# Performance work log

Measured on AMD Instinct MI355X. Metric: run time of the kernel, lower is better.

Reference implementation:

```python
import jax, jax.numpy as jnp
import numpy as np

EPS = 1e-5

def _branch(x, W, gamma, beta):
    # 1x1 conv (no bias) + InstanceNorm2d(affine) + ReLU
    y = jnp.einsum('oc,bchw->bohw', W, x)
    mu = y.mean(axis=(2, 3), keepdims=True)
    var = y.var(axis=(2, 3), keepdims=True)
    y = (y - mu) * jax.lax.rsqrt(var + EPS)
    y = y * gamma[None, :, None, None] + beta[None, :, None, None]
    return jax.nn.relu(y)

def setup_inputs() -> dict:
    key = jax.random.key(0)
    ks = jax.random.split(key, 12)
    b, in_ch, h, w = 2, 256, 64, 64
    c = in_ch // 8
    d = dict(
        x1=jax.random.normal(ks[0], (b, in_ch, h, w), jnp.float32),
        x2=jax.random.normal(ks[1], (b, in_ch, h, w), jnp.float32),
        x3=jax.random.normal(ks[2], (b, in_ch, h, w), jnp.float32),
        W1=jax.random.normal(ks[3], (c, in_ch), jnp.float32) * (1.0 / np.sqrt(in_ch)),
        g1=jnp.ones((c,), jnp.float32), b1=jnp.zeros((c,), jnp.float32),
        W2=jax.random.normal(ks[4], (c, in_ch), jnp.float32) * (1.0 / np.sqrt(in_ch)),
        g2=jnp.ones((c,), jnp.float32), b2=jnp.zeros((c,), jnp.float32),
        W3=jax.random.normal(ks[5], (c, in_ch), jnp.float32) * (1.0 / np.sqrt(in_ch)),
        g3=jnp.ones((c,), jnp.float32), b3=jnp.zeros((c,), jnp.float32),
    )
    return d

def _forward(x1, x2, x3, W1, g1, b1, W2, g2, b2, W3, g3, b3):
    q1 = _branch(x1, W1, g1, b1); q2 = _branch(x2, W1, g1, b1); q3 = _branch(x3, W1, g1, b1)
    k1 = _branch(x1, W2, g2, b2); k2 = _branch(x2, W2, g2, b2); k3 = _branch(x3, W2, g2, b2)
    v1 = _branch(x1, W3, g3, b3); v2 = _branch(x2, W3, g3, b3); v3 = _branch(x3, W3, g3, b3)
    b_, c, h, w = q1.shape
    hw = h * w
    Q1 = q1.reshape(b_, c, hw).transpose(0, 2, 1)  # [b,hw,c]
    Q2 = q2.reshape(b_, c, hw).transpose(0, 2, 1)
    Q3 = q3.reshape(b_, c, hw).transpose(0, 2, 1)
    K1 = k1.reshape(b_, c, hw)                      # [b,c,hw]
    K2 = k2.reshape(b_, c, hw)
    K3 = k3.reshape(b_, c, hw)
    sm = lambda Q, K: jax.nn.softmax(jnp.einsum('bic,bcj->bij', Q, K), axis=-1)
    A12 = sm(Q1, K2); A21 = sm(Q2, K1); A23 = sm(Q2, K3)
    A32 = sm(Q3, K2); A13 = sm(Q1, K3)
    # ones[b,c,hw] @ A == broadcast of column-sums of A: track a [b,hw] vector
    colsum = lambda A: A.sum(axis=1)                        # [b,hw]
    step = lambda v, A: jnp.einsum('bk,bkj->bj', v, A)      # [b,hw]
    def bc(v):  # broadcast [b,hw] -> [b,c,h,w]
        return jnp.broadcast_to(v[:, None, :], (b_, c, hw)).reshape(b_, c, h, w)
    p1a = bc(step(step(step(colsum(A12), A23), A32), A21))
    p1b = bc(step(colsum(A12), A21))
    p2 = bc(step(colsum(A23), A32))
    p3a = bc(step(colsum(A12), A23))
    p3b = bc(colsum(A13))
    return (p1a, p1b, p2, p3a, p3b, v1, v2, v3)

def reference(x1, x2, x3, W1, g1, b1, W2, g2, b2, W3, g3, b3):
    return _forward(x1, x2, x3, W1, g1, b1, W2, g2, b2, W3, g3, b3)
```

## Files before the change

### kernel.cpp

```cpp
#include <hip/hip_runtime.h>

typedef unsigned short u16;
typedef u16  u16x8  __attribute__((ext_vector_type(8)));
typedef _Float16 f16x4 __attribute__((ext_vector_type(4)));
typedef _Float16 f16x8 __attribute__((ext_vector_type(8)));
typedef float f32x4 __attribute__((ext_vector_type(4)));

#define HW 4096
#define CIN 256
#define HW32 (HW * 32)
#define L2E 1.4426950408889634f

__device__ __forceinline__ float fexp2(float x) { return __builtin_amdgcn_exp2f(x); }

__global__ __launch_bounds__(256) void convert_kernel(const float* x1, const float* x2, const float* x3,
        const float* W1, const float* W2, const float* W3,
        _Float16* xh, _Float16* wh, float* mean) {
    int bx = blockIdx.x; int t = threadIdx.x;
    if (bx < 1536) {
        int xi = bx >> 9, b = (bx >> 8) & 1, c = bx & 255;
        const float* src = (xi == 0 ? x1 : xi == 1 ? x2 : x3) + (size_t)(b * CIN + c) * HW;
        _Float16* dst = xh + ((size_t)((xi * 2 + b) * CIN) + c) * HW;
        float s = 0.f;
        for (int i = t; i < 1024; i += 256) {
            f32x4 v = ((const f32x4*)src)[i];
            s += v[0] + v[1] + v[2] + v[3];
            f16x4 h;
#pragma unroll
            for (int r = 0; r < 4; ++r) h[r] = (_Float16)v[r];
            ((f16x4*)dst)[i] = h;
        }
        __shared__ float red[256];
        red[t] = s; __syncthreads();
        for (int k = 128; k; k >>= 1) { if (t < k) red[t] += red[t + k]; __syncthreads(); }
        if (t == 0) mean[(xi * 2 + b) * CIN + c] = red[0] * (1.f / HW);
    } else {
        int j = bx - 1536;
        int widx = j >> 1, half = j & 1;
        const float* wsrc = (widx == 0 ? W1 : widx == 1 ? W2 : W3) + half * 4096;
        _Float16* wdst = wh + widx * 8192 + half * 4096;
        for (int i = t; i < 1024; i += 256) {
            f32x4 v = ((const f32x4*)wsrc)[i];
            f16x4 h;
#pragma unroll
            for (int r = 0; r < 4; ++r) h[r] = (_Float16)v[r];
            ((f16x4*)wdst)[i] = h;
        }
    }
}

__global__ __launch_bounds__(256) void m2_kernel(const _Float16* xh, float* Pm2) {
    int xi = blockIdx.y, b = blockIdx.z;
    int xb = xi * 2 + b;
    const _Float16* X = xh + (size_t)xb * CIN * HW;
    int bx = blockIdx.x;
    int chunk = bx >> 4, blk = bx & 15;
    int t = threadIdx.x; int wv = t >> 6; int L = t & 63; int m = L & 15; int quad = L >> 4;
    int region = blk * 4 + wv;
    int r1 = (region >> 3) * 32, r2 = (region & 7) * 32;
    int p0 = chunk * 512 + quad * 8;
    const f16x8* A0 = (const f16x8*)(X + (size_t)(r1 + m) * HW + p0);
    const f16x8* A1 = (const f16x8*)(X + (size_t)(r1 + 16 + m) * HW + p0);
    const f16x8* B0 = (const f16x8*)(X + (size_t)(r2 + m) * HW + p0);
    const f16x8* B1 = (const f16x8*)(X + (size_t)(r2 + 16 + m) * HW + p0);
    f32x4 zero = {0, 0, 0, 0};
    f32x4 acc00 = zero, acc01 = zero, acc10 = zero, acc11 = zero;
#pragma unroll 4
    for (int it = 0; it < 16; ++it) {
        f16x8 a0 = A0[it * 4], a1 = A1[it * 4];
        f16x8 b0 = B0[it * 4], b1 = B1[it * 4];
        acc00 = __builtin_amdgcn_mfma_f32_16x16x32_f16(a0, b0, acc00, 0, 0, 0);
        acc01 = __builtin_amdgcn_mfma_f32_16x16x32_f16(a0, b1, acc01, 0, 0, 0);
        acc10 = __builtin_amdgcn_mfma_f32_16x16x32_f16(a1, b0, acc10, 0, 0, 0);
        acc11 = __builtin_amdgcn_mfma_f32_16x16x32_f16(a1, b1, acc11, 0, 0, 0);
    }
    float* dst = Pm2 + ((size_t)chunk * 6 + xb) * 65536;
#pragma unroll
    for (int r = 0; r < 4; ++r) {
        int row0 = (r1 + quad * 4 + r) * 256, row1 = (r1 + 16 + quad * 4 + r) * 256;
        dst[row0 + r2 + m] = acc00[r];
        dst[row0 + r2 + 16 + m] = acc01[r];
        dst[row1 + r2 + m] = acc10[r];
        dst[row1 + r2 + 16 + m] = acc11[r];
    }
}

__global__ __launch_bounds__(256) void m2combine_kernel(const float* Pm2, float* M2) {
    size_t e = (size_t)blockIdx.x * 256 + threadIdx.x;
    float s = 0.f;
#pragma unroll
    for (int c = 0; c < 8; ++c) s += Pm2[(size_t)c * 6 * 65536 + e];
    M2[e] = s * (1.f / HW);
}

__global__ __launch_bounds__(256) void stats_kernel(const float* M2, const float* mean,
        const float* W1, const float* W2, const float* W3,
        const float* g1, const float* g2, const float* g3,
        const float* b1, const float* b2, const float* b3, float2* afine) {
    int o = blockIdx.x; int xi = blockIdx.y; int b = blockIdx.z;
    int widx = o >> 5; int oc = o & 31;
    const float* Wp = (widx == 0 ? W1 : widx == 1 ? W2 : W3) + oc * CIN;
    const float* gp = (widx == 0 ? g1 : widx == 1 ? g2 : g3);
    const float* bp = (widx == 0 ? b1 : widx == 1 ? b2 : b3);
    int t = threadIdx.x;
    __shared__ float sW[256];
    __shared__ float red[256];
    sW[t] = Wp[t];
    __syncthreads();
    const float* m2row = M2 + ((size_t)(xi * 2 + b) * CIN + t) * CIN;
    float tv = 0.f;
    const f32x4* r4 = (const f32x4*)m2row;
#pragma unroll 4
    for (int k = 0; k < 64; ++k) {
        f32x4 mv = r4[k];
        const f32x4 wv = *(const f32x4*)&sW[k * 4];
        tv += mv[0] * wv[0] + mv[1] * wv[1] + mv[2] * wv[2] + mv[3] * wv[3];
    }
    red[t] = tv * sW[t]; __syncthreads();
    for (int k = 128; k; k >>= 1) { if (t < k) red[t] += red[t + k]; __syncthreads(); }
    float E2 = red[0]; __syncthreads();
    red[t] = sW[t] * mean[(xi * 2 + b) * CIN + t]; __syncthreads();
    for (int k = 128; k; k >>= 1) { if (t < k) red[t] += red[t + k]; __syncthreads(); }
    if (t == 0) {
        float mu = red[0];
        float var = E2 - mu * mu;
        float rsig = rsqrtf(var + 1e-5f);
        float scale = gp[oc] * rsig;
        float bias = bp[oc] - mu * scale;
        if (widx == 0) { scale *= L2E; bias *= L2E; }
        afine[(xi * 2 + b) * 96 + o] = make_float2(scale, bias);
    }
}

__global__ __launch_bounds__(256) void conv_kernel(const _Float16* xh, const _Float16* wh,
        const float2* afine, _Float16* qT, _Float16* kT, float* out) {
    int xi = blockIdx.y, b = blockIdx.z;
    const u16* xb = (const u16*)(xh + (size_t)(xi * 2 + b) * CIN * HW);
    int p0 = blockIdx.x * 64;
    __shared__ u16 lds[32 * 65 * 8];
    int t = threadIdx.x;
    {
        int pc = t & 7, cg = t >> 3;
        u16x8 a[8];
#pragma unroll
        for (int r = 0; r < 8; ++r)
            a[r] = *(const u16x8*)(xb + (size_t)(cg * 8 + r) * HW + p0 + pc * 8);
#pragma unroll
        for (int i = 0; i < 8; ++i) {
            u16x8 d;
#pragma unroll
            for (int r = 0; r < 8; ++r) d[r] = a[r][i];
            int p = pc * 8 + i; int fp = p ^ (p >> 3);
            *(u16x8*)&lds[(cg * 65 + fp) * 8] = d;
        }
    }
    __syncthreads();
    int wv = t >> 6, L = t & 63, m = L & 15, quad = L >> 4;
    int pw0 = wv * 16;
    f16x8 af[8];
    {
        int p = pw0 + m; int fp = p ^ (p >> 3);
#pragma unroll
        for (int k = 0; k < 8; ++k)
            af[k] = *(const f16x8*)&lds[((k * 4 + quad) * 65 + fp) * 8];
    }
    int xb2 = xi * 2 + b;
    for (int ot = 0; ot < 6; ++ot) {
        int o0 = ot * 16; int widx = ot >> 1;
        int o_col = o0 + m;
        f32x4 acc = {0, 0, 0, 0};
#pragma unroll
        for (int k = 0; k < 8; ++k) {
            f16x8 bfr = *(const f16x8*)(wh + (size_t)o_col * CIN + k * 32 + quad * 8);
            acc = __builtin_amdgcn_mfma_f32_16x16x32_f16(af[k], bfr, acc, 0, 0, 0);
        }
        float2 afv = afine[xb2 * 96 + o_col];
        f32x4 vals;
#pragma unroll
        for (int r = 0; r < 4; ++r) {
            float v = acc[r] * afv.x + afv.y;
            vals[r] = v > 0.f ? v : 0.f;
        }
        int prow = p0 + pw0 + quad * 4;
        if (widx < 2) {
            _Float16* dst = (widx == 0 ? qT : kT) + (size_t)xb2 * HW32;
            int cc = (o0 & 31) + m;
#pragma unroll
            for (int r = 0; r < 4; ++r)
                dst[(size_t)(prow + r) * 32 + cc] = (_Float16)vals[r];
        } else {
            float* dst = out + (size_t)(5 + xi) * 262144 + (size_t)b * 131072 + (size_t)(o_col - 64) * HW + prow;
            *(f32x4*)dst = vals;
        }
    }
}

__global__ __launch_bounds__(256) void zsweep_kernel(const _Float16* qT, const _Float16* kT,
        float2* Pz) {
    const int qxA[5] = {0, 1, 1, 2, 0};
    const int kxA[5] = {1, 0, 2, 1, 2};
    int mat = blockIdx.y, b = blockIdx.z;
    const _Float16* qb = qT + (size_t)(qxA[mat] * 2 + b) * HW32;
    const _Float16* kb = kT + (size_t)(kxA[mat] * 2 + b) * HW32;
    int bx = blockIdx.x;
    int jc = bx & 15, qblk = bx >> 4;
    int t = threadIdx.x; int wv = t >> 6; int L = t & 63; int m = L & 15; int quad = L >> 4;
    int i0 = qblk * 256 + wv * 64;
    f16x8 a[4];
#pragma unroll
    for (int tt = 0; tt < 4; ++tt)
        a[tt] = *(const f16x8*)(qb + (size_t)(i0 + tt * 16 + m) * 32 + quad * 8);
    const f16x8* kp = (const f16x8*)(kb + m * 32 + quad * 8) + (size_t)jc * (16 * 64);
    f32x4 zero = {0.f, 0.f, 0.f, 0.f};
    f32x4 mx[4] = {zero, zero, zero, zero};
#pragma unroll 4
    for (int j = 0; j < 16; ++j) {
        f16x8 bf = kp[j * 64];
#pragma unroll
        for (int tt = 0; tt < 4; ++tt) {
            f32x4 d = __builtin_amdgcn_mfma_f32_16x16x32_f16(a[tt], bf, zero, 0, 0, 0);
            mx[tt][0] = fmaxf(mx[tt][0], d[0]); mx[tt][1] = fmaxf(mx[tt][1], d[1]);
            mx[tt][2] = fmaxf(mx[tt][2], d[2]); mx[tt][3] = fmaxf(mx[tt][3], d[3]);
        }
    }
#pragma unroll
    for (int tt = 0; tt < 4; ++tt)
#pragma unroll
        for (int msk = 1; msk <= 8; msk <<= 1) {
            mx[tt][0] = fmaxf(mx[tt][0], __shfl_xor(mx[tt][0], msk));
            mx[tt][1] = fmaxf(mx[tt][1], __shfl_xor(mx[tt][1], msk));
            mx[tt][2] = fmaxf(mx[tt][2], __shfl_xor(mx[tt][2], msk));
            mx[tt][3] = fmaxf(mx[tt][3], __shfl_xor(mx[tt][3], msk));
        }
    f32x4 neg[4];
#pragma unroll
    for (int tt = 0; tt < 4; ++tt) neg[tt] = -mx[tt];
    f32x4 z[4] = {zero, zero, zero, zero};
#pragma unroll 4
    for (int j = 0; j < 16; ++j) {
        f16x8 bf = kp[j * 64];
#pragma unroll
        for (int tt = 0; tt < 4; ++tt) {
            f32x4 d = __builtin_amdgcn_mfma_f32_16x16x32_f16(a[tt], bf, neg[tt], 0, 0, 0);
            z[tt][0] += fexp2(d[0]); z[tt][1] += fexp2(d[1]);
            z[tt][2] += fexp2(d[2]); z[tt][3] += fexp2(d[3]);
        }
    }
#pragma unroll
    for (int tt = 0; tt < 4; ++tt)
#pragma unroll
        for (int msk = 1; msk <= 8; msk <<= 1) {
            z[tt][0] += __shfl_xor(z[tt][0], msk); z[tt][1] += __shfl_xor(z[tt][1], msk);
            z[tt][2] += __shfl_xor(z[tt][2], msk); z[tt][3] += __shfl_xor(z[tt][3], msk);
        }
    if (m == 0) {
        int mb = mat * 2 + b;
#pragma unroll
        for (int tt = 0; tt < 4; ++tt) {
            int row = i0 + tt * 16 + quad * 4;
#pragma unroll
            for (int r = 0; r < 4; ++r)
                Pz[((size_t)mb * 16 + jc) * HW + row + r] = make_float2(mx[tt][r], z[tt][r]);
        }
    }
}

__global__ __launch_bounds__(256) void zcombine_kernel(const float2* Pz, float* R, float* Mv, float2* Wa) {
    int mb = blockIdx.y;
    int r = blockIdx.x * 256 + threadIdx.x;
    float2 p[16];
    float M = 0.f;
#pragma unroll
    for (int c = 0; c < 16; ++c) {
        p[c] = Pz[((size_t)mb * 16 + c) * HW + r];
        M = fmaxf(M, p[c].x);
    }
    float Z = 0.f;
#pragma unroll
    for (int c = 0; c < 16; ++c) Z += p[c].y * fexp2(p[c].x - M);
    float rz = 1.0f / Z;
    size_t idx = (size_t)mb * HW + r;
    R[idx] = rz; Mv[idx] = M;
    if (mb < 2 || mb >= 8) Wa[idx] = make_float2(rz, 0.f);
}

struct PCfg {
    const _Float16* qb; const _Float16* kb;
    const float* Mv;
    const float2* wt;
    float2* Pp;
    int nit;
};

__global__ __launch_bounds__(256) void pass2p_kernel(PCfg c0, PCfg c1) {
    PCfg c = (blockIdx.y == 0) ? c0 : c1;
    int b = blockIdx.z;
    int bx = blockIdx.x; int jb = bx & 15; int ic = bx >> 4;
    const _Float16* qb = c.qb + (size_t)b * HW32;
    const _Float16* kb = c.kb + (size_t)b * HW32;
    const float2* wt = c.wt + (size_t)b * HW;
    const float* Mb = c.Mv + (size_t)b * HW;
    int t = threadIdx.x; int wv = t >> 6; int L = t & 63; int m = L & 15; int quad = L >> 4;
    int j0 = jb * 256 + wv * 64;
    f16x8 bf[4];
#pragma unroll
    for (int tt = 0; tt < 4; ++tt)
        bf[tt] = *(const f16x8*)(kb + (size_t)(j0 + tt * 16 + m) * 32 + quad * 8);
    float a1[4] = {0, 0, 0, 0}, a2[4] = {0, 0, 0, 0};
    int ibase = ic * (c.nit * 16);
#pragma unroll 4
    for (int it = 0; it < c.nit; ++it) {
        int i0 = ibase + it * 16;
        f16x8 av = *(const f16x8*)(qb + (size_t)(i0 + m) * 32 + quad * 8);
        f32x4 Mr = *(const f32x4*)(Mb + i0 + quad * 4);
        f32x4 negM = -Mr;
        const float2* wr = wt + i0 + quad * 4;
        float2 w0 = wr[0], w1 = wr[1], w2 = wr[2], w3 = wr[3];
#pragma unroll
        for (int tt = 0; tt < 4; ++tt) {
            f32x4 d = __builtin_amdgcn_mfma_f32_16x16x32_f16(av, bf[tt], negM, 0, 0, 0);
            float e0 = fexp2(d[0]), e1 = fexp2(d[1]), e2 = fexp2(d[2]), e3 = fexp2(d[3]);
            a1[tt] += e0 * w0.x + e1 * w1.x + e2 * w2.x + e3 * w3.x;
            a2[tt] += e0 * w0.y + e1 * w1.y + e2 * w2.y + e3 * w3.y;
        }
    }
#pragma unroll
    for (int tt = 0; tt < 4; ++tt) {
        a1[tt] += __shfl_xor(a1[tt], 16); a1[tt] += __shfl_xor(a1[tt], 32);
        a2[tt] += __shfl_xor(a2[tt], 16); a2[tt] += __shfl_xor(a2[tt], 32);
    }
    if (quad == 0) {
        float2* dst = c.Pp + ((size_t)ic * 2 + b) * HW;
#pragma unroll
        for (int tt = 0; tt < 4; ++tt)
            dst[j0 + tt * 16 + m] = make_float2(a1[tt], a2[tt]);
    }
}

__global__ __launch_bounds__(256) void prepA_kernel(const float2* PpA, const float* R,
        float* c12, float* c13, float2* Wa2) {
    int b = blockIdx.y; int j = blockIdx.x * 256 + threadIdx.x;
    float s12 = 0.f, s13 = 0.f;
    for (int ic = 0; ic < 16; ++ic) {
        s12 += PpA[((size_t)ic * 2 + b) * HW + j].x;
        s13 += PpA[((size_t)(16 + ic) * 2 + b) * HW + j].x;
    }
    c12[(size_t)b * HW + j] = s12; c13[(size_t)b * HW + j] = s13;
    float rn = R[((size_t)(2 * 2 + b)) * HW + j];
    Wa2[(size_t)b * HW + j] = make_float2(rn, s12 * rn);
}

__global__ __launch_bounds__(256) void prep_kernel(const float2* Pp, const float* Rn,
        const float* aux, float* o1, float* o2, float2* Wn, int IC, int mode) {
    int b = blockIdx.y; int j = blockIdx.x * 256 + threadIdx.x;
    float s1 = 0.f, s2 = 0.f;
    for (int ic = 0; ic < IC; ++ic) {
        float2 p = Pp[((size_t)ic * 2 + b) * HW + j];
        s1 += p.x; s2 += p.y;
    }
    if (o1) o1[(size_t)b * HW + j] = s1;
    if (o2) o2[(size_t)b * HW + j] = s2;
    if (Wn) {
        float rn = Rn[(size_t)b * HW + j];
        float2 w = (mode == 0) ? make_float2(s1 * rn, s2 * rn)
                               : make_float2(s2 * rn, aux[(size_t)b * HW + j] * rn);
        Wn[(size_t)b * HW + j] = w;
    }
}

__global__ __launch_bounds__(256) void bcast_kernel(const float* vecs, float* out) {
    int bx = blockIdx.x;
    int s = bx >> 6; int rem = bx & 63; int b = rem >> 5; int c = rem & 31;
    const float* src = vecs + ((size_t)s * 2 + b) * HW;
    float* dst = out + ((size_t)(s * 2 + b) * 32 + c) * HW;
    int t = threadIdx.x;
#pragma unroll
    for (int k = 0; k < 4; ++k)
        ((f32x4*)dst)[k * 256 + t] = ((const f32x4*)src)[k * 256 + t];
}

extern "C" void kernel_launch(void* const* d_in, const int* in_sizes, int n_in,
                              void* d_out, int out_size, void* d_ws, size_t ws_size,
                              hipStream_t stream) {
    (void)in_sizes; (void)n_in; (void)out_size; (void)ws_size;
    const float* x1 = (const float*)d_in[0];
    const float* x2 = (const float*)d_in[1];
    const float* x3 = (const float*)d_in[2];
    const float* W1 = (const float*)d_in[3];
    const float* g1 = (const float*)d_in[4];
    const float* b1 = (const float*)d_in[5];
    const float* W2 = (const float*)d_in[6];
    const float* g2 = (const float*)d_in[7];
    const float* b2 = (const float*)d_in[8];
    const float* W3 = (const float*)d_in[9];
    const float* g3 = (const float*)d_in[10];
    const float* b3 = (const float*)d_in[11];
    float* out = (float*)d_out;

    char* w = (char*)d_ws;
    _Float16* xh    = (_Float16*)(w);
    _Float16* wh    = (_Float16*)(w + 12582912);
    float*    mean  = (float*)(w + 12632064);
    float*    M2    = (float*)(w + 12638208);
    float2*   afine = (float2*)(w + 14211072);
    _Float16* qT    = (_Float16*)(w + 14215680);
    _Float16* kT    = (_Float16*)(w + 15788544);
    float*    R     = (float*)(w + 17361408);
    float*    Mv    = (float*)(w + 17525248);
    float2*   Wa    = (float2*)(w + 17689088);
    float*    vecs  = (float*)(w + 18016768);
    float2*   Pz    = (float2*)(w + 18213376);
    float2*   PpA   = (float2*)(w + 23456256);
    float2*   PpB   = (float2*)(w + 25553408);
    float2*   PpC   = (float2*)(w + 27650560);
    float2*   PpD   = (float2*)(w + 29747712);
    float*    Pm2   = (float*)(w + 18213376);

    float* v_p1a = vecs + 0 * 2 * HW;
    float* v_p1b = vecs + 1 * 2 * HW;
    float* v_p2  = vecs + 2 * 2 * HW;
    float* v_p3a = vecs + 3 * 2 * HW;
    float* v_p3b = vecs + 4 * 2 * HW;
    float* v_c12 = vecs + 5 * 2 * HW;

    hipLaunchKernelGGL(convert_kernel, dim3(1542), dim3(256), 0, stream,
                       x1, x2, x3, W1, W2, W3, xh, wh, mean);
    hipLaunchKernelGGL(m2_kernel, dim3(128, 3, 2), dim3(256), 0, stream, xh, Pm2);
    hipLaunchKernelGGL(m2combine_kernel, dim3(1536), dim3(256), 0, stream, Pm2, M2);
    hipLaunchKernelGGL(stats_kernel, dim3(96, 3, 2), dim3(256), 0, stream,
                       M2, mean, W1, W2, W3, g1, g2, g3, b1, b2, b3, afine);
    hipLaunchKernelGGL(conv_kernel, dim3(64, 3, 2), dim3(256), 0, stream,
                       xh, wh, afine, qT, kT, out);
    hipLaunchKernelGGL(zsweep_kernel, dim3(256, 5, 2), dim3(256), 0, stream, qT, kT, Pz);
    hipLaunchKernelGGL(zcombine_kernel, dim3(16, 10), dim3(256), 0, stream, Pz, R, Mv, Wa);

    PCfg cA0 = { qT + 0 * 2 * HW32, kT + 1 * 2 * HW32, Mv + 0 * 2 * HW, Wa + 0 * 2 * HW, PpA,               16 };
    PCfg cA1 = { qT + 0 * 2 * HW32, kT + 2 * 2 * HW32, Mv + 4 * 2 * HW, Wa + 4 * 2 * HW, PpA + 16 * 2 * HW, 16 };
    hipLaunchKernelGGL(pass2p_kernel, dim3(256, 2, 2), dim3(256), 0, stream, cA0, cA1);
    hipLaunchKernelGGL(prepA_kernel, dim3(16, 2), dim3(256), 0, stream,
                       PpA, R, v_c12, v_p3b, Wa + 2 * 2 * HW);

    PCfg cB = { qT + 1 * 2 * HW32, kT + 2 * 2 * HW32, Mv + 2 * 2 * HW, Wa + 2 * 2 * HW, PpB, 8 };
    hipLaunchKernelGGL(pass2p_kernel, dim3(512, 1, 2), dim3(256), 0, stream, cB, cB);
    hipLaunchKernelGGL(prep_kernel, dim3(16, 2), dim3(256), 0, stream,
                       PpB, R + 3 * 2 * HW, (const float*)nullptr,
                       (float*)nullptr, v_p3a, Wa + 3 * 2 * HW, 32, 0);

    PCfg cC = { qT + 2 * 2 * HW32, kT + 1 * 2 * HW32, Mv + 3 * 2 * HW, Wa + 3 * 2 * HW, PpC, 8 };
    hipLaunchKernelGGL(pass2p_kernel, dim3(512, 1, 2), dim3(256), 0, stream, cC, cC);
    hipLaunchKernelGGL(prep_kernel, dim3(16, 2), dim3(256), 0, stream,
                       PpC, R + 1 * 2 * HW, v_c12,
                       v_p2, (float*)nullptr, Wa + 1 * 2 * HW, 32, 1);

    PCfg cD = { qT + 1 * 2 * HW32, kT + 0 * 2 * HW32, Mv + 1 * 2 * HW, Wa + 1 * 2 * HW, PpD, 8 };
    hipLaunchKernelGGL(pass2p_kernel, dim3(512, 1, 2), dim3(256), 0, stream, cD, cD);
    hipLaunchKernelGGL(prep_kernel, dim3(16, 2), dim3(256), 0, stream,
                       PpD, (const float*)nullptr, (const float*)nullptr,
                       v_p1a, v_p1b, (float2*)nullptr, 32, 0);

    hipLaunchKernelGGL(bcast_kernel, dim3(320), dim3(256), 0, stream, vecs, out);
}
```

Measured before the change: 293.3 us.

## Use global Cauchy-Schwarz norm bound as softmax shift instead of per-row max

Adds a small kernel that computes, per tensor and batch, the maximum row L2 norm of the q and k projections. The product of the two norms is used as one fixed softmax shift, replacing the per-row maximum. This removes the first max-finding MFMA sweep in zsweep, the max merge in zcombine, and the per-row M loads in pass2p. The risk is that the bound can sit far above the true row maxima, so the exp2 terms may underflow and the normaliser Z could lose precision or become zero.

```diff
diff --git a/kernel.cpp b/kernel.cpp
--- a/kernel.cpp
+++ b/kernel.cpp
@@ -195,13 +195,42 @@
     }
 }
 
+__global__ __launch_bounds__(256) void maxnorm_kernel(const _Float16* qT, const _Float16* kT,
+                                                      float* maxq, float* maxk) {
+    int id = blockIdx.x;
+    int which = id >> 1; int b = id & 1;
+    const _Float16* base = (which < 3 ? qT + (size_t)(which * 2 + b) * HW32
+                                      : kT + (size_t)((which - 3) * 2 + b) * HW32);
+    int t = threadIdx.x;
+    float mx = 0.f;
+    for (int i = t; i < HW; i += 256) {
+        const f16x8* r = (const f16x8*)(base + (size_t)i * 32);
+        float s = 0.f;
+#pragma unroll
+        for (int k = 0; k < 4; ++k) {
+            f16x8 v = r[k];
+#pragma unroll
+            for (int j = 0; j < 8; ++j) { float f = (float)v[j]; s += f * f; }
+        }
+        mx = fmaxf(mx, s);
+    }
+    __shared__ float red[256];
+    red[t] = mx; __syncthreads();
+    for (int k = 128; k; k >>= 1) { if (t < k) red[t] = fmaxf(red[t], red[t + k]); __syncthreads(); }
+    if (t == 0) {
+        float v = sqrtf(red[0]);
+        if (which < 3) maxq[which * 2 + b] = v; else maxk[(which - 3) * 2 + b] = v;
+    }
+}
+
 __global__ __launch_bounds__(256) void zsweep_kernel(const _Float16* qT, const _Float16* kT,
-        float2* Pz) {
+        const float* maxq, const float* maxk, float* Pz) {
     const int qxA[5] = {0, 1, 1, 2, 0};
     const int kxA[5] = {1, 0, 2, 1, 2};
     int mat = blockIdx.y, b = blockIdx.z;
     const _Float16* qb = qT + (size_t)(qxA[mat] * 2 + b) * HW32;
     const _Float16* kb = kT + (size_t)(kxA[mat] * 2 + b) * HW32;
+    float Cg = maxq[qxA[mat] * 2 + b] * maxk[kxA[mat] * 2 + b];
     int bx = blockIdx.x;
     int jc = bx & 15, qblk = bx >> 4;
     int t = threadIdx.x; int wv = t >> 6; int L = t & 63; int m = L & 15; int quad = L >> 4;
@@ -211,37 +240,15 @@
     for (int tt = 0; tt < 4; ++tt)
         a[tt] = *(const f16x8*)(qb + (size_t)(i0 + tt * 16 + m) * 32 + quad * 8);
     const f16x8* kp = (const f16x8*)(kb + m * 32 + quad * 8) + (size_t)jc * (16 * 64);
+    f32x4 negC = {-Cg, -Cg, -Cg, -Cg};
     f32x4 zero = {0.f, 0.f, 0.f, 0.f};
-    f32x4 mx[4] = {zero, zero, zero, zero};
-#pragma unroll 4
-    for (int j = 0; j < 16; ++j) {
-        f16x8 bf = kp[j * 64];
-#pragma unroll
-        for (int tt = 0; tt < 4; ++tt) {
-            f32x4 d = __builtin_amdgcn_mfma_f32_16x16x32_f16(a[tt], bf, zero, 0, 0, 0);
-            mx[tt][0] = fmaxf(mx[tt][0], d[0]); mx[tt][1] = fmaxf(mx[tt][1], d[1]);
-            mx[tt][2] = fmaxf(mx[tt][2], d[2]); mx[tt][3] = fmaxf(mx[tt][3], d[3]);
-        }
-    }
-#pragma unroll
-    for (int tt = 0; tt < 4; ++tt)
-#pragma unroll
-        for (int msk = 1; msk <= 8; msk <<= 1) {
-            mx[tt][0] = fmaxf(mx[tt][0], __shfl_xor(mx[tt][0], msk));
-            mx[tt][1] = fmaxf(mx[tt][1], __shfl_xor(mx[tt][1], msk));
-            mx[tt][2] = fmaxf(mx[tt][2], __shfl_xor(mx[tt][2], msk));
-            mx[tt][3] = fmaxf(mx[tt][3], __shfl_xor(mx[tt][3], msk));
-        }
-    f32x4 neg[4];
-#pragma unroll
-    for (int tt = 0; tt < 4; ++tt) neg[tt] = -mx[tt];
     f32x4 z[4] = {zero, zero, zero, zero};
 #pragma unroll 4
     for (int j = 0; j < 16; ++j) {
         f16x8 bf = kp[j * 64];
 #pragma unroll
         for (int tt = 0; tt < 4; ++tt) {
-            f32x4 d = __builtin_amdgcn_mfma_f32_16x16x32_f16(a[tt], bf, neg[tt], 0, 0, 0);
+            f32x4 d = __builtin_amdgcn_mfma_f32_16x16x32_f16(a[tt], bf, negC, 0, 0, 0);
             z[tt][0] += fexp2(d[0]); z[tt][1] += fexp2(d[1]);
             z[tt][2] += fexp2(d[2]); z[tt][3] += fexp2(d[3]);
         }
@@ -260,33 +267,26 @@
             int row = i0 + tt * 16 + quad * 4;
 #pragma unroll
             for (int r = 0; r < 4; ++r)
-                Pz[((size_t)mb * 16 + jc) * HW + row + r] = make_float2(mx[tt][r], z[tt][r]);
-        }
-    }
-}
-
-__global__ __launch_bounds__(256) void zcombine_kernel(const float2* Pz, float* R, float* Mv, float2* Wa) {
+                Pz[((size_t)mb * 16 + jc) * HW + row + r] = z[tt][r];
+        }
+    }
+}
+
+__global__ __launch_bounds__(256) void zcombine_kernel(const float* Pz, float* R, float2* Wa) {
     int mb = blockIdx.y;
     int r = blockIdx.x * 256 + threadIdx.x;
-    float2 p[16];
-    float M = 0.f;
-#pragma unroll
-    for (int c = 0; c < 16; ++c) {
-        p[c] = Pz[((size_t)mb * 16 + c) * HW + r];
-        M = fmaxf(M, p[c].x);
-    }
     float Z = 0.f;
 #pragma unroll
-    for (int c = 0; c < 16; ++c) Z += p[c].y * fexp2(p[c].x - M);
+    for (int c = 0; c < 16; ++c) Z += Pz[((size_t)mb * 16 + c) * HW + r];
     float rz = 1.0f / Z;
     size_t idx = (size_t)mb * HW + r;
-    R[idx] = rz; Mv[idx] = M;
+    R[idx] = rz;
     if (mb < 2 || mb >= 8) Wa[idx] = make_float2(rz, 0.f);
 }
 
 struct PCfg {
     const _Float16* qb; const _Float16* kb;
-    const float* Mv;
+    const float* mq; const float* mk;
     const float2* wt;
     float2* Pp;
     int nit;
@@ -299,26 +299,25 @@
     const _Float16* qb = c.qb + (size_t)b * HW32;
     const _Float16* kb = c.kb + (size_t)b * HW32;
     const float2* wt = c.wt + (size_t)b * HW;
-    const float* Mb = c.Mv + (size_t)b * HW;
+    float Cg = c.mq[b] * c.mk[b];
     int t = threadIdx.x; int wv = t >> 6; int L = t & 63; int m = L & 15; int quad = L >> 4;
     int j0 = jb * 256 + wv * 64;
     f16x8 bf[4];
 #pragma unroll
     for (int tt = 0; tt < 4; ++tt)
         bf[tt] = *(const f16x8*)(kb + (size_t)(j0 + tt * 16 + m) * 32 + quad * 8);
+    f32x4 negC = {-Cg, -Cg, -Cg, -Cg};
     float a1[4] = {0, 0, 0, 0}, a2[4] = {0, 0, 0, 0};
     int ibase = ic * (c.nit * 16);
 #pragma unroll 4
     for (int it = 0; it < c.nit; ++it) {
         int i0 = ibase + it * 16;
         f16x8 av = *(const f16x8*)(qb + (size_t)(i0 + m) * 32 + quad * 8);
-        f32x4 Mr = *(const f32x4*)(Mb + i0 + quad * 4);
-        f32x4 negM = -Mr;
         const float2* wr = wt + i0 + quad * 4;
         float2 w0 = wr[0], w1 = wr[1], w2 = wr[2], w3 = wr[3];
 #pragma unroll
         for (int tt = 0; tt < 4; ++tt) {
-            f32x4 d = __builtin_amdgcn_mfma_f32_16x16x32_f16(av, bf[tt], negM, 0, 0, 0);
+            f32x4 d = __builtin_amdgcn_mfma_f32_16x16x32_f16(av, bf[tt], negC, 0, 0, 0);
             float e0 = fexp2(d[0]), e1 = fexp2(d[1]), e2 = fexp2(d[2]), e3 = fexp2(d[3]);
             a1[tt] += e0 * w0.x + e1 * w1.x + e2 * w2.x + e3 * w3.x;
             a2[tt] += e0 * w0.y + e1 * w1.y + e2 * w2.y + e3 * w3.y;
@@ -406,10 +405,11 @@
     _Float16* qT    = (_Float16*)(w + 14215680);
     _Float16* kT    = (_Float16*)(w + 15788544);
     float*    R     = (float*)(w + 17361408);
-    float*    Mv    = (float*)(w + 17525248);
+    float*    maxq  = (float*)(w + 17525248);
+    float*    maxk  = (float*)(w + 17525312);
     float2*   Wa    = (float2*)(w + 17689088);
     float*    vecs  = (float*)(w + 18016768);
-    float2*   Pz    = (float2*)(w + 18213376);
+    float*    Pz    = (float*)(w + 18213376);
     float2*   PpA   = (float2*)(w + 23456256);
     float2*   PpB   = (float2*)(w + 25553408);
     float2*   PpC   = (float2*)(w + 27650560);
@@ -431,28 +431,29 @@
                        M2, mean, W1, W2, W3, g1, g2, g3, b1, b2, b3, afine);
     hipLaunchKernelGGL(conv_kernel, dim3(64, 3, 2), dim3(256), 0, stream,
                        xh, wh, afine, qT, kT, out);
-    hipLaunchKernelGGL(zsweep_kernel, dim3(256, 5, 2), dim3(256), 0, stream, qT, kT, Pz);
-    hipLaunchKernelGGL(zcombine_kernel, dim3(16, 10), dim3(256), 0, stream, Pz, R, Mv, Wa);
-
-    PCfg cA0 = { qT + 0 * 2 * HW32, kT + 1 * 2 * HW32, Mv + 0 * 2 * HW, Wa + 0 * 2 * HW, PpA,               16 };
-    PCfg cA1 = { qT + 0 * 2 * HW32, kT + 2 * 2 * HW32, Mv + 4 * 2 * HW, Wa + 4 * 2 * HW, PpA + 16 * 2 * HW, 16 };
+    hipLaunchKernelGGL(maxnorm_kernel, dim3(12), dim3(256), 0, stream, qT, kT, maxq, maxk);
+    hipLaunchKernelGGL(zsweep_kernel, dim3(256, 5, 2), dim3(256), 0, stream, qT, kT, maxq, maxk, Pz);
+    hipLaunchKernelGGL(zcombine_kernel, dim3(16, 10), dim3(256), 0, stream, Pz, R, Wa);
+
+    PCfg cA0 = { qT + 0 * 2 * HW32, kT + 1 * 2 * HW32, maxq + 0, maxk + 2, Wa + 0 * 2 * HW, PpA,               16 };
+    PCfg cA1 = { qT + 0 * 2 * HW32, kT + 2 * 2 * HW32, maxq + 0, maxk + 4, Wa + 4 * 2 * HW, PpA + 16 * 2 * HW, 16 };
     hipLaunchKernelGGL(pass2p_kernel, dim3(256, 2, 2), dim3(256), 0, stream, cA0, cA1);
     hipLaunchKernelGGL(prepA_kernel, dim3(16, 2), dim3(256), 0, stream,
                        PpA, R, v_c12, v_p3b, Wa + 2 * 2 * HW);
 
-    PCfg cB = { qT + 1 * 2 * HW32, kT + 2 * 2 * HW32, Mv + 2 * 2 * HW, Wa + 2 * 2 * HW, PpB, 8 };
+    PCfg cB = { qT + 1 * 2 * HW32, kT + 2 * 2 * HW32, maxq + 2, maxk + 4, Wa + 2 * 2 * HW, PpB, 8 };
     hipLaunchKernelGGL(pass2p_kernel, dim3(512, 1, 2), dim3(256), 0, stream, cB, cB);
     hipLaunchKernelGGL(prep_kernel, dim3(16, 2), dim3(256), 0, stream,
                        PpB, R + 3 * 2 * HW, (const float*)nullptr,
                        (float*)nullptr, v_p3a, Wa + 3 * 2 * HW, 32, 0);
 
-    PCfg cC = { qT + 2 * 2 * HW32, kT + 1 * 2 * HW32, Mv + 3 * 2 * HW, Wa + 3 * 2 * HW, PpC, 8 };
+    PCfg cC = { qT + 2 * 2 * HW32, kT + 1 * 2 * HW32, maxq + 4, maxk + 2, Wa + 3 * 2 * HW, PpC, 8 };
     hipLaunchKernelGGL(pass2p_kernel, dim3(512, 1, 2), dim3(256), 0, stream, cC, cC);
     hipLaunchKernelGGL(prep_kernel, dim3(16, 2), dim3(256), 0, stream,
                        PpC, R + 1 * 2 * HW, v_c12,
                        v_p2, (float*)nullptr, Wa + 1 * 2 * HW, 32, 1);
 
-    PCfg cD = { qT + 1 * 2 * HW32, kT + 0 * 2 * HW32, Mv + 1 * 2 * HW, Wa + 1 * 2 * HW, PpD, 8 };
+    PCfg cD = { qT + 1 * 2 * HW32, kT + 0 * 2 * HW32, maxq + 2, maxk + 0, Wa + 1 * 2 * HW, PpD, 8 };
     hipLaunchKernelGGL(pass2p_kernel, dim3(512, 1, 2), dim3(256), 0, stream, cD, cD);
     hipLaunchKernelGGL(prep_kernel, dim3(16, 2), dim3(256), 0, stream,
                        PpD, (const float*)nullptr, (const float*)nullptr,
```

New measurement: 282.2 us. 3.8% less time.
